# Performance work log

Hardware: AMD Instinct MI355X
Metric: run time of the kernel (lower is better)

## Reference

```python
import jax, jax.numpy as jnp
import numpy as np

EPS = 1e-5  # torch BatchNorm1d default
N_BLOCKS = 15


def setup_inputs() -> dict:
    key = jax.random.key(0)
    ks = jax.random.split(key, 5)
    B = 131072
    x = jax.random.normal(ks[0], (B, 29), dtype=jnp.float32)
    # first block params (Linear(29,59) + BN(59))
    W0 = jax.random.normal(ks[1], (59, 29), dtype=jnp.float32) * (1.0 / np.sqrt(29))
    b0 = jnp.zeros((59,), dtype=jnp.float32)
    g0 = jnp.ones((59,), dtype=jnp.float32)
    bt0 = jnp.zeros((59,), dtype=jnp.float32)
    # remaining 14 blocks (Linear(59,59) + BN(59)), stacked
    Ws = jax.random.normal(ks[2], (14, 59, 59), dtype=jnp.float32) * (1.0 / np.sqrt(59))
    bs = jnp.zeros((14, 59), dtype=jnp.float32)
    gs = jnp.ones((14, 59), dtype=jnp.float32)
    bts = jnp.zeros((14, 59), dtype=jnp.float32)
    return {"x": x, "W0": W0, "b0": b0, "g0": g0, "bt0": bt0,
            "Ws": Ws, "bs": bs, "gs": gs, "bts": bts}


def _block(x, W, b, g, bt):
    # Linear -> ReLU -> BatchNorm1d (training mode: batch stats, biased var)
    h = jnp.maximum(x @ W.T + b, 0.0)          # [B, 59]
    mu = jnp.mean(h, axis=0)                    # [59]
    var = jnp.mean((h - mu) ** 2, axis=0)       # biased variance
    return (h - mu) * jax.lax.rsqrt(var + EPS) * g + bt


def reference(x, W0, b0, g0, bt0, Ws, bs, gs, bts):
    h = _block(x, W0, b0, g0, bt0)

    def step(carry, p):
        W, b, g, bt = p
        return _block(carry, W, b, g, bt), None

    h, _ = jax.lax.scan(step, h, (Ws, bs, gs, bts))
    return h
```

## Files before the change

### kernel.cpp

```cpp
#include <hip/hip_runtime.h>

#define NTHR  256
#define F     59
#define K0    29
#define NB    15
#define B     131072
#define RPB   64
#define NBLK  (B / RPB)
#define NSLC  32
#define FPW   16
#define YSTR  66
#define KC0   32
#define KCN   60

#define ACC_PER_LAYER (F * NSLC * 2)
#define ACC_TOTAL     (NB * ACC_PER_LAYER)
#define WT_OFF_B      ((size_t)ACC_TOTAL * 8)
#define WT0_FLOATS    (KC0 * 64)
#define WTN_FLOATS    (KCN * 64)
#define WT_FLOATS     (WT0_FLOATS + 14 * WTN_FLOATS)
#define BP_OFF_B      (WT_OFF_B + (size_t)WT_FLOATS * 4)
#define HB_OFF_B      (BP_OFF_B + (size_t)NB * 64 * 4)

__global__ void transpose_w(const float* __restrict__ W0, const float* __restrict__ b0,
                            const float* __restrict__ Ws,
                            float* __restrict__ Wt, float* __restrict__ bp0)
{
  const int b = blockIdx.x;
  if (b == 0) {
    for (int i = threadIdx.x; i < KC0 * 64; i += blockDim.x) {
      int k = i >> 6, j = i & 63;
      Wt[i] = (k < K0 && j < F) ? W0[j * K0 + k] : 0.f;
    }
    if (threadIdx.x < 64) bp0[threadIdx.x] = (threadIdx.x < F) ? b0[threadIdx.x] : 0.f;
  } else {
    float* dst = Wt + WT0_FLOATS + (size_t)(b - 1) * WTN_FLOATS;
    const float* W = Ws + (size_t)(b - 1) * F * F;
    for (int i = threadIdx.x; i < KCN * 64; i += blockDim.x) {
      int k = i >> 6, j = i & 63;
      dst[i] = (k < F && j < F) ? W[j * F + k] : 0.f;
    }
  }
}

__global__ void fuse_w(const double* __restrict__ acc_prev,
                       const float* __restrict__ g, const float* __restrict__ bt,
                       const float* __restrict__ bias,
                       float* Wp, float* __restrict__ bp)
{
  __shared__ float  scf[64];
  __shared__ double shd[64];
  const int j = threadIdx.x;

  if (j < F) {
    const double* p = acc_prev + (size_t)j * (NSLC * 2);
    double s1 = 0.0, s2 = 0.0;
    #pragma unroll
    for (int s = 0; s < NSLC; ++s) { s1 += p[2 * s]; s2 += p[2 * s + 1]; }
    const double inv = 1.0 / (double)B;
    double mu   = s1 * inv;
    double var  = fma(s2, inv, -mu * mu);
    double rstd = 1.0 / sqrt(var + 1e-5);
    double sc   = rstd * (double)g[j];
    scf[j] = (float)sc;
    shd[j] = fma(-mu, sc, (double)bt[j]);
  } else { scf[j] = 0.f; shd[j] = 0.0; }
  __syncthreads();

  double bacc = (j < F) ? (double)bias[j] : 0.0;
  for (int k = 0; k < F; ++k) {
    float w = Wp[k * 64 + j];
    bacc = fma((double)w, shd[k], bacc);
    Wp[k * 64 + j] = w * scf[k];
  }
  bp[j] = (float)bacc;
}

__device__ __forceinline__ void scsh_wave0(const double* __restrict__ acc_prev,
                                           const float* __restrict__ g,
                                           const float* __restrict__ bt,
                                           float2* scsh, int lane)
{
  if (lane < F) {
    const double* p = acc_prev + (size_t)lane * (NSLC * 2);
    double s1 = 0.0, s2 = 0.0;
    #pragma unroll
    for (int s = 0; s < NSLC; ++s) { s1 += p[2 * s]; s2 += p[2 * s + 1]; }
    const double inv = 1.0 / (double)B;
    double mu   = s1 * inv;
    double var  = fma(s2, inv, -mu * mu);
    double rstd = 1.0 / sqrt(var + 1e-5);
    double sc   = rstd * (double)g[lane];
    scsh[lane] = make_float2((float)sc, (float)fma(-mu, sc, (double)bt[lane]));
  }
}

template<bool FIRST>
__global__ void __launch_bounds__(NTHR, 8)
layer_kernel(const float* __restrict__ in, const float* __restrict__ Wp,
             const float* __restrict__ bp,
             float* __restrict__ hout, double* acc)
{
  __shared__ __attribute__((aligned(16))) float lds[4 * FPW * YSTR];

  const int tid   = threadIdx.x;
  const int lane  = tid & 63;
  const int qu    = __builtin_amdgcn_readfirstlane(tid >> 6);
  const int rowbase = blockIdx.x * RPB;
  const int slice   = blockIdx.x & (NSLC - 1);

  if (FIRST) {
    for (int i = tid; i < RPB * 33; i += NTHR) {
      int r = i / 33, k = i - r * 33;
      lds[i] = (k < K0) ? in[(size_t)(rowbase + r) * K0 + k] : 0.f;
    }
    __syncthreads();
  }

  const int fbase = qu * FPW;
  const float* bq = bp + fbase;
  float a0=bq[0],a1=bq[1],a2=bq[2],a3=bq[3],a4=bq[4],a5=bq[5],a6=bq[6],a7=bq[7],
        a8=bq[8],a9=bq[9],a10=bq[10],a11=bq[11],a12=bq[12],a13=bq[13],a14=bq[14],a15=bq[15];

  #define FMA16(hk, wk)                                                     \
    a0  = fmaf(hk, (wk)[0],  a0);  a1  = fmaf(hk, (wk)[1],  a1);            \
    a2  = fmaf(hk, (wk)[2],  a2);  a3  = fmaf(hk, (wk)[3],  a3);            \
    a4  = fmaf(hk, (wk)[4],  a4);  a5  = fmaf(hk, (wk)[5],  a5);            \
    a6  = fmaf(hk, (wk)[6],  a6);  a7  = fmaf(hk, (wk)[7],  a7);            \
    a8  = fmaf(hk, (wk)[8],  a8);  a9  = fmaf(hk, (wk)[9],  a9);            \
    a10 = fmaf(hk, (wk)[10], a10); a11 = fmaf(hk, (wk)[11], a11);           \
    a12 = fmaf(hk, (wk)[12], a12); a13 = fmaf(hk, (wk)[13], a13);           \
    a14 = fmaf(hk, (wk)[14], a14); a15 = fmaf(hk, (wk)[15], a15);

  if (FIRST) {
    const float* hrow = lds + lane * 33;
    #pragma unroll 2
    for (int c = 0; c < 7; ++c) {
      float h0 = hrow[4*c], h1 = hrow[4*c+1], h2 = hrow[4*c+2], h3 = hrow[4*c+3];
      const float* wk = Wp + (size_t)(4 * c) * 64 + fbase;
      FMA16(h0, wk) FMA16(h1, wk + 64) FMA16(h2, wk + 128) FMA16(h3, wk + 192)
    }
    { float h28 = hrow[28];
      FMA16(h28, Wp + (size_t)28 * 64 + fbase) }
    __syncthreads();
  } else {
    const float* hcol = in + rowbase + lane;
    #pragma unroll 2
    for (int c = 0; c < 14; ++c) {
      float h0 = hcol[(size_t)(4*c)   * B];
      float h1 = hcol[(size_t)(4*c+1) * B];
      float h2 = hcol[(size_t)(4*c+2) * B];
      float h3 = hcol[(size_t)(4*c+3) * B];
      const float* wk = Wp + (size_t)(4 * c) * 64 + fbase;
      FMA16(h0, wk) FMA16(h1, wk + 64) FMA16(h2, wk + 128) FMA16(h3, wk + 192)
    }
    { float h56 = hcol[(size_t)56 * B];
      float h57 = hcol[(size_t)57 * B];
      float h58 = hcol[(size_t)58 * B];
      const float* wk = Wp + (size_t)56 * 64 + fbase;
      FMA16(h56, wk) FMA16(h57, wk + 64) FMA16(h58, wk + 128) }
  }
  #undef FMA16

  a0=fmaxf(a0,0.f); a1=fmaxf(a1,0.f); a2=fmaxf(a2,0.f); a3=fmaxf(a3,0.f);
  a4=fmaxf(a4,0.f); a5=fmaxf(a5,0.f); a6=fmaxf(a6,0.f); a7=fmaxf(a7,0.f);
  a8=fmaxf(a8,0.f); a9=fmaxf(a9,0.f); a10=fmaxf(a10,0.f); a11=fmaxf(a11,0.f);
  a12=fmaxf(a12,0.f); a13=fmaxf(a13,0.f); a14=fmaxf(a14,0.f); a15=fmaxf(a15,0.f);

  float* op = hout + rowbase + lane;
  #define ST(j, aj) if (fbase + j < F) op[(size_t)(fbase + j) * B] = aj;
  ST(0,a0)  ST(1,a1)  ST(2,a2)  ST(3,a3)  ST(4,a4)  ST(5,a5)  ST(6,a6)  ST(7,a7)
  ST(8,a8)  ST(9,a9)  ST(10,a10) ST(11,a11) ST(12,a12) ST(13,a13) ST(14,a14) ST(15,a15)
  #undef ST

  float* ytq = lds + qu * (FPW * YSTR);
  ytq[0*YSTR+lane]=a0;   ytq[1*YSTR+lane]=a1;   ytq[2*YSTR+lane]=a2;
  ytq[3*YSTR+lane]=a3;   ytq[4*YSTR+lane]=a4;   ytq[5*YSTR+lane]=a5;
  ytq[6*YSTR+lane]=a6;   ytq[7*YSTR+lane]=a7;   ytq[8*YSTR+lane]=a8;
  ytq[9*YSTR+lane]=a9;   ytq[10*YSTR+lane]=a10; ytq[11*YSTR+lane]=a11;
  ytq[12*YSTR+lane]=a12; ytq[13*YSTR+lane]=a13; ytq[14*YSTR+lane]=a14;
  ytq[15*YSTR+lane]=a15;

  const int fl = lane >> 2, c = lane & 3;
  const float* yp = ytq + fl * YSTR + c * 16;
  float4 v0 = *(const float4*)(yp);
  float4 v1 = *(const float4*)(yp + 4);
  float4 v2 = *(const float4*)(yp + 8);
  float4 v3 = *(const float4*)(yp + 12);
  float s1 = ((v0.x+v0.y)+(v0.z+v0.w)) + ((v1.x+v1.y)+(v1.z+v1.w))
           + ((v2.x+v2.y)+(v2.z+v2.w)) + ((v3.x+v3.y)+(v3.z+v3.w));
  float s2 = 0.f;
  s2=fmaf(v0.x,v0.x,s2); s2=fmaf(v0.y,v0.y,s2); s2=fmaf(v0.z,v0.z,s2); s2=fmaf(v0.w,v0.w,s2);
  s2=fmaf(v1.x,v1.x,s2); s2=fmaf(v1.y,v1.y,s2); s2=fmaf(v1.z,v1.z,s2); s2=fmaf(v1.w,v1.w,s2);
  s2=fmaf(v2.x,v2.x,s2); s2=fmaf(v2.y,v2.y,s2); s2=fmaf(v2.z,v2.z,s2); s2=fmaf(v2.w,v2.w,s2);
  s2=fmaf(v3.x,v3.x,s2); s2=fmaf(v3.y,v3.y,s2); s2=fmaf(v3.z,v3.z,s2); s2=fmaf(v3.w,v3.w,s2);

  s1 += __shfl_xor(s1, 1, 64);  s2 += __shfl_xor(s2, 1, 64);
  s1 += __shfl_xor(s1, 2, 64);  s2 += __shfl_xor(s2, 2, 64);

  if (c == 0 && fbase + fl < F) {
    double* slot = acc + ((size_t)(fbase + fl) * NSLC + slice) * 2;
    atomicAdd(slot,     (double)s1);
    atomicAdd(slot + 1, (double)s2);
  }
}

__global__ void __launch_bounds__(NTHR, 8)
final_tr_kernel(const float* __restrict__ hT, const double* __restrict__ acc_last,
                const float* __restrict__ g, const float* __restrict__ bt,
                float* __restrict__ out)
{
  __shared__ float2 scsh[64];
  __shared__ float  ybuf[F * 64];
  const int tid  = threadIdx.x;
  const int lane = tid & 63;
  const int qu   = __builtin_amdgcn_readfirstlane(tid >> 6);
  const int rowbase = blockIdx.x * RPB;

  if (qu == 0) {
    scsh_wave0(acc_last, g, bt, scsh, lane);
  } else {
    for (int i = tid - 64; i < F * 16; i += (NTHR - 64)) {
      int j = i >> 4, r4 = i & 15;
      float4 v = *(const float4*)(hT + (size_t)j * B + rowbase + r4 * 4);
      *(float4*)&ybuf[j * 64 + r4 * 4] = v;
    }
  }
  __syncthreads();

  float* oblk = out + (size_t)rowbase * F;
  for (int i = tid; i < RPB * F; i += NTHR) {
    int r = i / F, j = i - r * F;
    float2 s = scsh[j];
    oblk[i] = fmaf(ybuf[j * 64 + r], s.x, s.y);
  }
}

extern "C" void kernel_launch(void* const* d_in, const int* in_sizes, int n_in,
                              void* d_out, int out_size, void* d_ws, size_t ws_size,
                              hipStream_t stream)
{
  const float* x   = (const float*)d_in[0];
  const float* W0  = (const float*)d_in[1];
  const float* b0  = (const float*)d_in[2];
  const float* g0  = (const float*)d_in[3];
  const float* bt0 = (const float*)d_in[4];
  const float* Ws  = (const float*)d_in[5];
  const float* bs  = (const float*)d_in[6];
  const float* gs  = (const float*)d_in[7];
  const float* bts = (const float*)d_in[8];
  float* out = (float*)d_out;

  double* acc = (double*)d_ws;
  float*  Wt  = (float*)((char*)d_ws + WT_OFF_B);
  float*  bp  = (float*)((char*)d_ws + BP_OFF_B);
  float*  hB  = (float*)((char*)d_ws + HB_OFF_B);
  float*  hA  = out;

  hipMemsetAsync(d_ws, 0, (size_t)ACC_TOTAL * sizeof(double), stream);

  transpose_w<<<NB, NTHR, 0, stream>>>(W0, b0, Ws, Wt, bp);

  layer_kernel<true><<<NBLK, NTHR, 0, stream>>>(x, Wt, bp, hB, acc);

  for (int b = 1; b < NB; ++b) {
    const float* gp  = (b == 1) ? g0  : gs  + (size_t)(b - 2) * F;
    const float* btp = (b == 1) ? bt0 : bts + (size_t)(b - 2) * F;
    float* Wpb = Wt + WT0_FLOATS + (size_t)(b - 1) * WTN_FLOATS;
    fuse_w<<<1, 64, 0, stream>>>(acc + (size_t)(b - 1) * ACC_PER_LAYER,
                                 gp, btp, bs + (size_t)(b - 1) * F,
                                 Wpb, bp + (size_t)b * 64);
    const float* src = (b & 1) ? hB : hA;
    float*       dst = (b & 1) ? hA : hB;
    layer_kernel<false><<<NBLK, NTHR, 0, stream>>>(
        src, Wpb, bp + (size_t)b * 64, dst, acc + (size_t)b * ACC_PER_LAYER);
  }

  final_tr_kernel<<<NBLK, NTHR, 0, stream>>>(
      hB, acc + (size_t)(NB - 1) * ACC_PER_LAYER,
      gs + (size_t)(NB - 2) * F, bts + (size_t)(NB - 2) * F, out);
}
```

Baseline: 431.0 us.

## Fold BatchNorm apply into next layer's input load, drop fuse_w kernels

Removes the 14 single-block fuse_w launches that folded BN scale and shift into weights. Each layer block now recomputes per-feature scale/shift from the previous layer's atomic accumulators, using 4 threads per feature and shuffles. It then applies them as one FMA per loaded input element before the matmul. The number of atomic slices drops from 32 to 8, so each block reads fewer partial sums but atomic contention rises. Every block redundantly does the stats reduction, and the final kernel uses all waves for loading.

```diff
diff --git a/kernel.cpp b/kernel.cpp
--- a/kernel.cpp
+++ b/kernel.cpp
@@ -7,7 +7,7 @@
 #define B     131072
 #define RPB   64
 #define NBLK  (B / RPB)
-#define NSLC  32
+#define NSLC  8
 #define FPW   16
 #define YSTR  66
 #define KC0   32
@@ -23,8 +23,8 @@
 #define HB_OFF_B      (BP_OFF_B + (size_t)NB * 64 * 4)
 
 __global__ void transpose_w(const float* __restrict__ W0, const float* __restrict__ b0,
-                            const float* __restrict__ Ws,
-                            float* __restrict__ Wt, float* __restrict__ bp0)
+                            const float* __restrict__ Ws, const float* __restrict__ bs,
+                            float* __restrict__ Wt, float* __restrict__ bp)
 {
   const int b = blockIdx.x;
   if (b == 0) {
@@ -32,7 +32,8 @@
       int k = i >> 6, j = i & 63;
       Wt[i] = (k < K0 && j < F) ? W0[j * K0 + k] : 0.f;
     }
-    if (threadIdx.x < 64) bp0[threadIdx.x] = (threadIdx.x < F) ? b0[threadIdx.x] : 0.f;
+    if (threadIdx.x < 64)
+      bp[threadIdx.x] = (threadIdx.x < F) ? b0[threadIdx.x] : 0.f;
   } else {
     float* dst = Wt + WT0_FLOATS + (size_t)(b - 1) * WTN_FLOATS;
     const float* W = Ws + (size_t)(b - 1) * F * F;
@@ -40,58 +41,33 @@
       int k = i >> 6, j = i & 63;
       dst[i] = (k < F && j < F) ? W[j * F + k] : 0.f;
     }
-  }
-}
-
-__global__ void fuse_w(const double* __restrict__ acc_prev,
-                       const float* __restrict__ g, const float* __restrict__ bt,
-                       const float* __restrict__ bias,
-                       float* Wp, float* __restrict__ bp)
-{
-  __shared__ float  scf[64];
-  __shared__ double shd[64];
-  const int j = threadIdx.x;
-
-  if (j < F) {
-    const double* p = acc_prev + (size_t)j * (NSLC * 2);
-    double s1 = 0.0, s2 = 0.0;
-    #pragma unroll
-    for (int s = 0; s < NSLC; ++s) { s1 += p[2 * s]; s2 += p[2 * s + 1]; }
-    const double inv = 1.0 / (double)B;
-    double mu   = s1 * inv;
-    double var  = fma(s2, inv, -mu * mu);
-    double rstd = 1.0 / sqrt(var + 1e-5);
-    double sc   = rstd * (double)g[j];
-    scf[j] = (float)sc;
-    shd[j] = fma(-mu, sc, (double)bt[j]);
-  } else { scf[j] = 0.f; shd[j] = 0.0; }
-  __syncthreads();
-
-  double bacc = (j < F) ? (double)bias[j] : 0.0;
-  for (int k = 0; k < F; ++k) {
-    float w = Wp[k * 64 + j];
-    bacc = fma((double)w, shd[k], bacc);
-    Wp[k * 64 + j] = w * scf[k];
-  }
-  bp[j] = (float)bacc;
-}
-
-__device__ __forceinline__ void scsh_wave0(const double* __restrict__ acc_prev,
-                                           const float* __restrict__ g,
-                                           const float* __restrict__ bt,
-                                           float2* scsh, int lane)
-{
-  if (lane < F) {
-    const double* p = acc_prev + (size_t)lane * (NSLC * 2);
-    double s1 = 0.0, s2 = 0.0;
-    #pragma unroll
-    for (int s = 0; s < NSLC; ++s) { s1 += p[2 * s]; s2 += p[2 * s + 1]; }
-    const double inv = 1.0 / (double)B;
-    double mu   = s1 * inv;
-    double var  = fma(s2, inv, -mu * mu);
-    double rstd = 1.0 / sqrt(var + 1e-5);
-    double sc   = rstd * (double)g[lane];
-    scsh[lane] = make_float2((float)sc, (float)fma(-mu, sc, (double)bt[lane]));
+    if (threadIdx.x < 64) {
+      int j = threadIdx.x;
+      bp[b * 64 + j] = (j < F) ? bs[(size_t)(b - 1) * F + j] : 0.f;
+    }
+  }
+}
+
+__device__ __forceinline__ void scsh_parallel(const double* __restrict__ acc_prev,
+                                              const float* __restrict__ g,
+                                              const float* __restrict__ bt,
+                                              float2* scsh, int tid)
+{
+  if (tid < 4 * F) {
+    const int j = tid >> 2, c = tid & 3;
+    const double* p = acc_prev + (size_t)j * (NSLC * 2) + c * 4;
+    double s1 = p[0] + p[2];
+    double s2 = p[1] + p[3];
+    s1 += __shfl_xor(s1, 1, 64);  s2 += __shfl_xor(s2, 1, 64);
+    s1 += __shfl_xor(s1, 2, 64);  s2 += __shfl_xor(s2, 2, 64);
+    if (c == 0) {
+      const double inv = 1.0 / (double)B;
+      double mu   = s1 * inv;
+      double var  = fma(s2, inv, -mu * mu);
+      double rstd = 1.0 / sqrt(var + 1e-5);
+      double sc   = rstd * (double)g[j];
+      scsh[j] = make_float2((float)sc, (float)fma(-mu, sc, (double)bt[j]));
+    }
   }
 }
 
@@ -99,9 +75,12 @@
 __global__ void __launch_bounds__(NTHR, 8)
 layer_kernel(const float* __restrict__ in, const float* __restrict__ Wp,
              const float* __restrict__ bp,
+             const double* __restrict__ acc_prev,
+             const float* __restrict__ g_prev, const float* __restrict__ bt_prev,
              float* __restrict__ hout, double* acc)
 {
   __shared__ __attribute__((aligned(16))) float lds[4 * FPW * YSTR];
+  __shared__ __attribute__((aligned(16))) float2 scsh[64];
 
   const int tid   = threadIdx.x;
   const int lane  = tid & 63;
@@ -114,6 +93,9 @@
       int r = i / 33, k = i - r * 33;
       lds[i] = (k < K0) ? in[(size_t)(rowbase + r) * K0 + k] : 0.f;
     }
+    __syncthreads();
+  } else {
+    scsh_parallel(acc_prev, g_prev, bt_prev, scsh, tid);
     __syncthreads();
   }
 
@@ -147,16 +129,20 @@
     const float* hcol = in + rowbase + lane;
     #pragma unroll 2
     for (int c = 0; c < 14; ++c) {
-      float h0 = hcol[(size_t)(4*c)   * B];
-      float h1 = hcol[(size_t)(4*c+1) * B];
-      float h2 = hcol[(size_t)(4*c+2) * B];
-      float h3 = hcol[(size_t)(4*c+3) * B];
+      float4 sA = *(const float4*)&scsh[4*c];
+      float4 sB = *(const float4*)&scsh[4*c+2];
+      float h0 = fmaf(hcol[(size_t)(4*c)   * B], sA.x, sA.y);
+      float h1 = fmaf(hcol[(size_t)(4*c+1) * B], sA.z, sA.w);
+      float h2 = fmaf(hcol[(size_t)(4*c+2) * B], sB.x, sB.y);
+      float h3 = fmaf(hcol[(size_t)(4*c+3) * B], sB.z, sB.w);
       const float* wk = Wp + (size_t)(4 * c) * 64 + fbase;
       FMA16(h0, wk) FMA16(h1, wk + 64) FMA16(h2, wk + 128) FMA16(h3, wk + 192)
     }
-    { float h56 = hcol[(size_t)56 * B];
-      float h57 = hcol[(size_t)57 * B];
-      float h58 = hcol[(size_t)58 * B];
+    { float4 sA = *(const float4*)&scsh[56];
+      float2 sC = scsh[58];
+      float h56 = fmaf(hcol[(size_t)56 * B], sA.x, sA.y);
+      float h57 = fmaf(hcol[(size_t)57 * B], sA.z, sA.w);
+      float h58 = fmaf(hcol[(size_t)58 * B], sC.x, sC.y);
       const float* wk = Wp + (size_t)56 * 64 + fbase;
       FMA16(h56, wk) FMA16(h57, wk + 64) FMA16(h58, wk + 128) }
   }
@@ -212,19 +198,14 @@
 {
   __shared__ float2 scsh[64];
   __shared__ float  ybuf[F * 64];
-  const int tid  = threadIdx.x;
-  const int lane = tid & 63;
-  const int qu   = __builtin_amdgcn_readfirstlane(tid >> 6);
+  const int tid = threadIdx.x;
   const int rowbase = blockIdx.x * RPB;
 
-  if (qu == 0) {
-    scsh_wave0(acc_last, g, bt, scsh, lane);
-  } else {
-    for (int i = tid - 64; i < F * 16; i += (NTHR - 64)) {
-      int j = i >> 4, r4 = i & 15;
-      float4 v = *(const float4*)(hT + (size_t)j * B + rowbase + r4 * 4);
-      *(float4*)&ybuf[j * 64 + r4 * 4] = v;
-    }
+  scsh_parallel(acc_last, g, bt, scsh, tid);
+  for (int i = tid; i < F * 16; i += NTHR) {
+    int j = i >> 4, r4 = i & 15;
+    float4 v = *(const float4*)(hT + (size_t)j * B + rowbase + r4 * 4);
+    *(float4*)&ybuf[j * 64 + r4 * 4] = v;
   }
   __syncthreads();
 
@@ -259,21 +240,21 @@
 
   hipMemsetAsync(d_ws, 0, (size_t)ACC_TOTAL * sizeof(double), stream);
 
-  transpose_w<<<NB, NTHR, 0, stream>>>(W0, b0, Ws, Wt, bp);
-
-  layer_kernel<true><<<NBLK, NTHR, 0, stream>>>(x, Wt, bp, hB, acc);
+  transpose_w<<<NB, NTHR, 0, stream>>>(W0, b0, Ws, bs, Wt, bp);
+
+  layer_kernel<true><<<NBLK, NTHR, 0, stream>>>(
+      x, Wt, bp, nullptr, nullptr, nullptr, hB, acc);
 
   for (int b = 1; b < NB; ++b) {
     const float* gp  = (b == 1) ? g0  : gs  + (size_t)(b - 2) * F;
     const float* btp = (b == 1) ? bt0 : bts + (size_t)(b - 2) * F;
-    float* Wpb = Wt + WT0_FLOATS + (size_t)(b - 1) * WTN_FLOATS;
-    fuse_w<<<1, 64, 0, stream>>>(acc + (size_t)(b - 1) * ACC_PER_LAYER,
-                                 gp, btp, bs + (size_t)(b - 1) * F,
-                                 Wpb, bp + (size_t)b * 64);
+    const float* Wpb = Wt + WT0_FLOATS + (size_t)(b - 1) * WTN_FLOATS;
     const float* src = (b & 1) ? hB : hA;
     float*       dst = (b & 1) ? hA : hB;
     layer_kernel<false><<<NBLK, NTHR, 0, stream>>>(
-        src, Wpb, bp + (size_t)b * 64, dst, acc + (size_t)b * ACC_PER_LAYER);
+        src, Wpb, bp + (size_t)b * 64,
+        acc + (size_t)(b - 1) * ACC_PER_LAYER, gp, btp,
+        dst, acc + (size_t)b * ACC_PER_LAYER);
   }
 
   final_tr_kernel<<<NBLK, NTHR, 0, stream>>>(
```

New measurement: 910.7 us. +111.3%, slower.
